# Optimization experiments

Hardware: AMD Instinct MI355X
Metric: run time of the kernel (lower is better)

## Reference

```python
import jax, jax.numpy as jnp
import numpy as np
import math

B, L, WIN, D, H, FF, NL, V, M = 16, 2048, 128, 512, 8, 2048, 3, 32000, 32
HD = D // H
EPS = 1e-5
RECON_W = 0.1

def _ln(x, g, b):
    m = x.mean(-1, keepdims=True)
    v = ((x - m) ** 2).mean(-1, keepdims=True)
    return (x - m) * jax.lax.rsqrt(v + EPS) * g + b

def _denoiser(x_t, t, motif, left, right, glob, time_proj_W, time_proj_b, cond_proj_W, cond_proj_b,
              qkv_W, qkv_b, attn_out_W, attn_out_b, ff1_W, ff1_b, ff2_W, ff2_b,
              ln1_g, ln1_b, ln2_g, ln2_b, out_W, out_b):
    half = D // 2
    freqs = jnp.exp(-math.log(10000.0) * jnp.arange(half) / (half - 1))
    a = t[:, None] * freqs[None, :]
    temb = jnp.concatenate([jnp.sin(a), jnp.cos(a)], -1) @ time_proj_W.T + time_proj_b
    x = x_t + temb[:, None, :]
    cond = jnp.concatenate([motif, left, right, glob], -1) @ cond_proj_W.T + cond_proj_b
    x = jnp.concatenate([cond[:, None, :], x], 1)
    S = x.shape[1]
    for i in range(NL):  # post-norm TransformerEncoderLayer, relu, no dropout (eval)
        qkv = x @ qkv_W[i].T + qkv_b[i]
        q, k, v = jnp.split(qkv, 3, axis=-1)
        q = q.reshape(B, S, H, HD); k = k.reshape(B, S, H, HD); v = v.reshape(B, S, H, HD)
        attn = jax.nn.softmax(jnp.einsum('bqhd,bkhd->bhqk', q, k) / math.sqrt(HD), axis=-1)
        ctx = jnp.einsum('bhqk,bkhd->bqhd', attn, v).reshape(B, S, D)
        x = _ln(x + ctx @ attn_out_W[i].T + attn_out_b[i], ln1_g[i], ln1_b[i])
        h = jax.nn.relu(x @ ff1_W[i].T + ff1_b[i]) @ ff2_W[i].T + ff2_b[i]
        x = _ln(x + h, ln2_g[i], ln2_b[i])
    return x[:, 1:, :] @ out_W.T + out_b

def setup_inputs():
    key = jax.random.key(0)
    ks = jax.random.split(key, 20)
    s = 0.02
    inp = {}
    inp['token_ids'] = jax.random.randint(ks[0], (B, L), 0, V)
    inp['motif_ids'] = jax.random.randint(ks[1], (B, M), 0, V)
    inp['motif_len'] = jax.random.randint(ks[2], (B,), 1, M + 1)
    inp['window_start'] = jax.random.randint(ks[3], (B,), 0, L - WIN)
    lens = jax.random.randint(ks[4], (B,), 1, WIN + 1).at[0].set(WIN)
    inp['window_end'] = inp['window_start'] + lens
    inp['t'] = jax.random.uniform(ks[5], (B,))
    inp['x0'] = jax.random.normal(ks[6], (B, WIN, D))
    inp['embed_table'] = jax.random.normal(ks[7], (V, D)) * s
    inp['decode_W'] = jax.random.normal(ks[8], (V, D)) * s
    inp['decode_b'] = jnp.zeros((V,))
    inp['adapter_W'] = jax.random.normal(ks[9], (D, D)) * s
    inp['adapter_b'] = jnp.zeros((D,))
    inp['time_proj_W'] = jax.random.normal(ks[10], (D, D)) * s
    inp['time_proj_b'] = jnp.zeros((D,))
    inp['cond_proj_W'] = jax.random.normal(ks[11], (D, 4 * D)) * s
    inp['cond_proj_b'] = jnp.zeros((D,))
    inp['qkv_W'] = jax.random.normal(ks[12], (NL, 3 * D, D)) * s
    inp['qkv_b'] = jnp.zeros((NL, 3 * D))
    inp['attn_out_W'] = jax.random.normal(ks[13], (NL, D, D)) * s
    inp['attn_out_b'] = jnp.zeros((NL, D))
    inp['ff1_W'] = jax.random.normal(ks[14], (NL, FF, D)) * s
    inp['ff1_b'] = jnp.zeros((NL, FF))
    inp['ff2_W'] = jax.random.normal(ks[15], (NL, D, FF)) * s
    inp['ff2_b'] = jnp.zeros((NL, D))
    inp['ln1_g'] = jnp.ones((NL, D)); inp['ln1_b'] = jnp.zeros((NL, D))
    inp['ln2_g'] = jnp.ones((NL, D)); inp['ln2_b'] = jnp.zeros((NL, D))
    inp['out_W'] = jax.random.normal(ks[16], (D, D)) * s
    inp['out_b'] = jnp.zeros((D,))
    return inp

def _forward(token_ids, motif_ids, motif_len, window_start, window_end, t, x0,
             embed_table, decode_W, decode_b, adapter_W, adapter_b, den):
    hidden = embed_table[token_ids]  # frozen backbone encode: [B, L, D]
    pos = jnp.arange(L)
    def pool(s, e):  # vectorized masked mean over region [s, e)
        m = ((pos[None, :] >= s[:, None]) & (pos[None, :] < e[:, None])).astype(hidden.dtype)
        return jnp.einsum('bl,bld->bd', m, hidden) / jnp.maximum(m.sum(1, keepdims=True), 1.0)
    left = pool(jnp.zeros_like(window_start), window_start)
    right = pool(window_end, jnp.full_like(window_end, L))
    glob = hidden.mean(1)
    memb = embed_table[motif_ids]
    mmask = (jnp.arange(M)[None, :] < motif_len[:, None]).astype(memb.dtype)
    motif = (memb * mmask[..., None]).sum(1) / jnp.maximum(motif_len.astype(memb.dtype), 1.0)[:, None]
    actual = jnp.clip(window_end - window_start, 0, WIN)
    win_mask = jnp.arange(WIN)[None, :] < actual[:, None]
    idx = jnp.clip(window_start[:, None] + jnp.arange(WIN)[None, :], 0, L - 1)
    x1 = jnp.take_along_axis(hidden, idx[:, :, None], axis=1) * win_mask[..., None]
    x_t = (1 - t[:, None, None]) * x0 + t[:, None, None] * x1
    target_v = x1 - x0
    pred_v = _denoiser(x_t, t, motif, left, right, glob, *den)
    valid = win_mask[..., None].astype(x1.dtype)
    vel = (((pred_v - target_v) ** 2) * valid).sum() / (jnp.maximum(valid.sum(), 1.0) * D)
    pred_x1 = x_t + (1 - t[:, None, None]) * pred_v
    logits = (pred_x1 @ adapter_W.T + adapter_b) @ decode_W.T + decode_b
    labels = jnp.where(win_mask, jnp.take_along_axis(token_ids, idx, axis=1), -100)
    lv = labels != -100
    logp = jax.nn.log_softmax(logits, axis=-1)
    picked = jnp.take_along_axis(logp, jnp.maximum(labels, 0)[..., None], axis=-1)[..., 0]
    recon = -(picked * lv).sum() / jnp.maximum(lv.sum(), 1)
    return vel + RECON_W * recon

def reference(token_ids, motif_ids, motif_len, window_start, window_end, t, x0,
              embed_table, decode_W, decode_b, adapter_W, adapter_b,
              time_proj_W, time_proj_b, cond_proj_W, cond_proj_b, qkv_W, qkv_b,
              attn_out_W, attn_out_b, ff1_W, ff1_b, ff2_W, ff2_b,
              ln1_g, ln1_b, ln2_g, ln2_b, out_W, out_b):
    den = (time_proj_W, time_proj_b, cond_proj_W, cond_proj_b, qkv_W, qkv_b,
           attn_out_W, attn_out_b, ff1_W, ff1_b, ff2_W, ff2_b,
           ln1_g, ln1_b, ln2_g, ln2_b, out_W, out_b)
    return _forward(token_ids, motif_ids, motif_len, window_start, window_end, t, x0,
                    embed_table, decode_W, decode_b, adapter_W, adapter_b, den)
```

## Files before the change

### kernel.cpp

```cpp
#include <hip/hip_runtime.h>
#include <hip/hip_bf16.h>
#include <math.h>

typedef __hip_bfloat16 bf16;

constexpr int cB = 16, cL = 2048, cWIN = 128, cD = 512, cH = 8, cFF = 2048;
constexpr int cNL = 3, cV = 32000, cM = 32;
constexpr int cHD = cD / cH;
constexpr int cS = cWIN + 1;
constexpr float cEPS = 1e-5f;
constexpr float cRECON_W = 0.1f;
constexpr int cNVT = cV / 128;

__device__ __forceinline__ float b2f(bf16 x) { return __bfloat162float(x); }

__device__ __forceinline__ float ldx(const void* p, size_t i, int f32) {
    return f32 ? ((const float*)p)[i]
               : __bfloat162float(((const bf16*)p)[i]);
}

__device__ __forceinline__ unsigned int f2bf(float f) {
    union { float f; unsigned int u; } v; v.f = f;
    unsigned int u = v.u + 0x7FFFu + ((v.u >> 16) & 1u);
    return u >> 16;
}

typedef short bf16x8 __attribute__((ext_vector_type(8)));
typedef float f32x4  __attribute__((ext_vector_type(4)));

__global__ void detect_kernel(const void* __restrict__ x0raw, int* __restrict__ flag)
{
    const unsigned short* h = (const unsigned short*)x0raw;
    int tid = threadIdx.x;
    int cnt = 0;
    for (int j = tid; j < 8192; j += 256) {
        unsigned short u = h[2 * j];
        int e = (u >> 7) & 0xFF;
        if (e >= 134) cnt++;
    }
    __shared__ int red[256];
    red[tid] = cnt; __syncthreads();
    for (int off = 128; off > 0; off >>= 1) {
        if (tid < off) red[tid] += red[tid + off];
        __syncthreads();
    }
    if (tid == 0) *flag = (red[0] > 400) ? 1 : 0;
}

__global__ __launch_bounds__(512) void pools_part_kernel(
    const int* __restrict__ tok, const int* __restrict__ wstart,
    const int* __restrict__ wend, const void* __restrict__ emb,
    float* __restrict__ part, const int* __restrict__ dflag)
{
    const int f32 = *dflag;
    int chunk = blockIdx.x;
    int b = blockIdx.y;
    int d = threadIdx.x;
    int ws_ = wstart[b], we_ = wend[b];
    float sl = 0.f, sr = 0.f, sg = 0.f;
    int l0 = chunk * 256;
    for (int l = l0; l < l0 + 256; ++l) {
        int t = tok[b * cL + l];
        float h = ldx(emb, (size_t)t * cD + d, f32);
        sg += h;
        if (l < ws_) sl += h;
        if (l >= we_) sr += h;
    }
    size_t base = ((size_t)(b * 8 + chunk)) * 3 * cD;
    part[base + d]            = sl;
    part[base + cD + d]       = sr;
    part[base + 2 * cD + d]   = sg;
}

__global__ __launch_bounds__(512) void pools_combine_kernel(
    const float* __restrict__ part, const int* __restrict__ mids,
    const int* __restrict__ mlen, const int* __restrict__ wstart,
    const int* __restrict__ wend, const void* __restrict__ emb,
    unsigned short* __restrict__ featb, const int* __restrict__ dflag)
{
    const int f32 = *dflag;
    int b = blockIdx.x;
    int d = threadIdx.x;
    int ws_ = wstart[b], we_ = wend[b];
    float sl = 0.f, sr = 0.f, sg = 0.f;
    for (int c = 0; c < 8; ++c) {
        size_t base = ((size_t)(b * 8 + c)) * 3 * cD;
        sl += part[base + d];
        sr += part[base + cD + d];
        sg += part[base + 2 * cD + d];
    }
    int ml = mlen[b];
    float sm = 0.f;
    for (int j = 0; j < cM; ++j) {
        if (j < ml) sm += ldx(emb, (size_t)mids[b * cM + j] * cD + d, f32);
    }
    unsigned short* fr = featb + (size_t)b * (4 * cD);
    fr[d]            = (unsigned short)f2bf(sm / fmaxf((float)ml, 1.f));
    fr[cD + d]       = (unsigned short)f2bf(sl / fmaxf((float)ws_, 1.f));
    fr[2 * cD + d]   = (unsigned short)f2bf(sr / fmaxf((float)(cL - we_), 1.f));
    fr[3 * cD + d]   = (unsigned short)f2bf(sg / (float)cL);
}

__global__ __launch_bounds__(512) void tf_kernel(
    const void* __restrict__ t_arr, unsigned short* __restrict__ tfbb,
    const int* __restrict__ dflag)
{
    const int f32 = *dflag;
    int b = blockIdx.x;
    int j = threadIdx.x;
    float t = ldx(t_arr, b, f32);
    const int half = cD / 2;
    float v;
    if (j < half) {
        float fr = expf(-logf(10000.f) * (float)j / (float)(half - 1));
        v = sinf(t * fr);
    } else {
        float fr = expf(-logf(10000.f) * (float)(j - half) / (float)(half - 1));
        v = cosf(t * fr);
    }
    tfbb[(size_t)b * cD + j] = (unsigned short)f2bf(v);
}

__global__ __launch_bounds__(512) void build_x_kernel(
    const int* __restrict__ tok, const int* __restrict__ wstart,
    const int* __restrict__ wend, const void* __restrict__ t_arr,
    const void* __restrict__ x0, const void* __restrict__ emb,
    const float* __restrict__ cond, const float* __restrict__ temb,
    float* __restrict__ x, unsigned short* __restrict__ xbf,
    float* __restrict__ x1, float* __restrict__ xt,
    const int* __restrict__ dflag)
{
    const int f32 = *dflag;
    int row = blockIdx.x;
    int b = row / cS, s = row % cS;
    int d = threadIdx.x;
    if (s == 0) {
        float cv = cond[b * cD + d];
        x[(size_t)row * cD + d] = cv;
        xbf[(size_t)row * cD + d] = (unsigned short)f2bf(cv);
        return;
    }
    int i = s - 1;
    int ws_ = wstart[b], we_ = wend[b];
    int actual = min(max(we_ - ws_, 0), cWIN);
    int idx = min(ws_ + i, cL - 1);
    float x1v = 0.f;
    if (i < actual) x1v = ldx(emb, (size_t)tok[b * cL + idx] * cD + d, f32);
    float t = ldx(t_arr, b, f32);
    float x0v = ldx(x0, ((size_t)b * cWIN + i) * cD + d, f32);
    float xtv = (1.f - t) * x0v + t * x1v;
    size_t ro = ((size_t)b * cWIN + i) * cD + d;
    x1[ro] = x1v;
    xt[ro] = xtv;
    float xv = xtv + temb[b * cD + d];
    x[(size_t)row * cD + d] = xv;
    xbf[(size_t)row * cD + d] = (unsigned short)f2bf(xv);
}

constexpr int GL2 = 72;
__global__ __launch_bounds__(256) void gemm_bf(
    const unsigned short* __restrict__ Abf, const void* __restrict__ Wb,
    size_t wOff, const void* __restrict__ biasb, size_t bOff,
    float* __restrict__ Cf, unsigned short* __restrict__ Cbf,
    int Mdim, int Ndim, int Kdim, int relu, int obf,
    const int* __restrict__ dflag)
{
    const int f32 = *dflag;
    const float* Wf = (const float*)Wb + wOff;
    const unsigned short* Wh = (const unsigned short*)Wb + wOff;
    __shared__ unsigned short As[2][64 * GL2];
    __shared__ unsigned short Bs[2][64 * GL2];
    const int tid = threadIdx.x;
    const int lane = tid & 63;
    const int wid = tid >> 6;
    const int wm = wid >> 1, wn = wid & 1;
    const int quad = lane >> 4, lm = lane & 15;
    const int m0 = blockIdx.y * 64;
    const int n0 = blockIdx.x * 64;

    f32x4 acc[2][2];
    #pragma unroll
    for (int i = 0; i < 2; ++i)
        #pragma unroll
        for (int j = 0; j < 2; ++j)
            acc[i][j] = (f32x4){0.f, 0.f, 0.f, 0.f};

    uint4 ra[2], rb[2];
    const int srow = tid >> 3;
    const int sc8  = (tid & 7) * 8;

    auto loadA = [&](int k0) {
        #pragma unroll
        for (int t = 0; t < 2; ++t) {
            int row = srow + t * 32;
            uint4 v = {0u, 0u, 0u, 0u};
            if (m0 + row < Mdim)
                v = *(const uint4*)(Abf + (size_t)(m0 + row) * Kdim + k0 + sc8);
            ra[t] = v;
        }
    };
    auto loadB = [&](int k0) {
        #pragma unroll
        for (int t = 0; t < 2; ++t) {
            int row = srow + t * 32;
            size_t g = (size_t)(n0 + row) * Kdim + k0 + sc8;
            if (f32) {
                float4 v0 = *(const float4*)(Wf + g);
                float4 v1 = *(const float4*)(Wf + g + 4);
                rb[t] = make_uint4(
                    f2bf(v0.x) | (f2bf(v0.y) << 16), f2bf(v0.z) | (f2bf(v0.w) << 16),
                    f2bf(v1.x) | (f2bf(v1.y) << 16), f2bf(v1.z) | (f2bf(v1.w) << 16));
            } else {
                rb[t] = *(const uint4*)(Wh + g);
            }
        }
    };

    loadA(0); loadB(0);
    const int nk = Kdim >> 6;
    for (int t = 0; t < nk; ++t) {
        const int buf = t & 1;
        #pragma unroll
        for (int u = 0; u < 2; ++u) {
            *(uint4*)(&As[buf][(srow + u * 32) * GL2 + sc8]) = ra[u];
            *(uint4*)(&Bs[buf][(srow + u * 32) * GL2 + sc8]) = rb[u];
        }
        __syncthreads();
        if (t + 1 < nk) { loadA((t + 1) * 64); loadB((t + 1) * 64); }
        #pragma unroll
        for (int kk = 0; kk < 2; ++kk) {
            bf16x8 a0 = *(const bf16x8*)(&As[buf][(wm * 32 + lm) * GL2 + kk * 32 + quad * 8]);
            bf16x8 a1 = *(const bf16x8*)(&As[buf][(wm * 32 + 16 + lm) * GL2 + kk * 32 + quad * 8]);
            bf16x8 b0 = *(const bf16x8*)(&Bs[buf][(wn * 32 + lm) * GL2 + kk * 32 + quad * 8]);
            bf16x8 b1 = *(const bf16x8*)(&Bs[buf][(wn * 32 + 16 + lm) * GL2 + kk * 32 + quad * 8]);
            acc[0][0] = __builtin_amdgcn_mfma_f32_16x16x32_bf16(a0, b0, acc[0][0], 0, 0, 0);
            acc[0][1] = __builtin_amdgcn_mfma_f32_16x16x32_bf16(a0, b1, acc[0][1], 0, 0, 0);
            acc[1][0] = __builtin_amdgcn_mfma_f32_16x16x32_bf16(a1, b0, acc[1][0], 0, 0, 0);
            acc[1][1] = __builtin_amdgcn_mfma_f32_16x16x32_bf16(a1, b1, acc[1][1], 0, 0, 0);
        }
    }

    #pragma unroll
    for (int in = 0; in < 2; ++in) {
        int gc = n0 + wn * 32 + in * 16 + lm;
        float bv = ldx(biasb, bOff + gc, f32);
        #pragma unroll
        for (int im = 0; im < 2; ++im) {
            #pragma unroll
            for (int r = 0; r < 4; ++r) {
                int gr = m0 + wm * 32 + im * 16 + quad * 4 + r;
                if (gr < Mdim) {
                    float v = acc[im][in][r] + bv;
                    if (relu) v = fmaxf(v, 0.f);
                    if (obf) Cbf[(size_t)gr * Ndim + gc] = (unsigned short)f2bf(v);
                    else     Cf[(size_t)gr * Ndim + gc] = v;
                }
            }
        }
    }
}

__global__ __launch_bounds__(256) void attn_mfma_kernel(
    const unsigned short* __restrict__ qkv, unsigned short* __restrict__ ctx)
{
    constexpr int SP = 160;
    constexpr int KP = 72;
    constexpr int VP = 168;
    const int h = blockIdx.x, b = blockIdx.y;
    const int tid = threadIdx.x;
    const int lane = tid & 63;
    const int wid = tid >> 6;
    const int quad = lane >> 4, lm = lane & 15;

    __shared__ unsigned short Ks[SP * KP];
    __shared__ unsigned short Vt[64 * VP];
    __shared__ unsigned short Pl[4 * 16 * VP];

    const unsigned short* base = qkv + (size_t)b * cS * (3 * cD) + h * cHD;

    for (int c = tid; c < SP * 8; c += 256) {
        int row = c >> 3, g = c & 7;
        uint4 v = {0u, 0u, 0u, 0u};
        if (row < cS)
            v = *(const uint4*)(base + (size_t)row * (3 * cD) + cD + g * 8);
        *(uint4*)(Ks + row * KP + g * 8) = v;
    }
    for (int c = tid; c < SP * 16; c += 256) {
        int key = c >> 4, d4 = c & 15;
        uint2 v = {0u, 0u};
        if (key < cS)
            v = *(const uint2*)(base + (size_t)key * (3 * cD) + 2 * cD + d4 * 4);
        Vt[(d4 * 4 + 0) * VP + key] = (unsigned short)(v.x & 0xFFFFu);
        Vt[(d4 * 4 + 1) * VP + key] = (unsigned short)(v.x >> 16);
        Vt[(d4 * 4 + 2) * VP + key] = (unsigned short)(v.y & 0xFFFFu);
        Vt[(d4 * 4 + 3) * VP + key] = (unsigned short)(v.y >> 16);
    }
    __syncthreads();

    unsigned short* Pw = Pl + wid * (16 * VP);

    for (int t = wid; t < 9; t += 4) {
        int qs = t * 16 + lm;
        bf16x8 aq[2];
        #pragma unroll
        for (int j = 0; j < 8; ++j) { aq[0][j] = 0; aq[1][j] = 0; }
        if (qs < cS) {
            const unsigned short* qrow = base + (size_t)qs * (3 * cD);
            aq[0] = *(const bf16x8*)(qrow + quad * 8);
            aq[1] = *(const bf16x8*)(qrow + 32 + quad * 8);
        }

        f32x4 sc[10];
        #pragma unroll
        for (int n = 0; n < 10; ++n) {
            sc[n] = (f32x4){0.f, 0.f, 0.f, 0.f};
            bf16x8 bk0 = *(const bf16x8*)(Ks + (n * 16 + lm) * KP + quad * 8);
            sc[n] = __builtin_amdgcn_mfma_f32_16x16x32_bf16(aq[0], bk0, sc[n], 0, 0, 0);
            bf16x8 bk1 = *(const bf16x8*)(Ks + (n * 16 + lm) * KP + 32 + quad * 8);
            sc[n] = __builtin_amdgcn_mfma_f32_16x16x32_bf16(aq[1], bk1, sc[n], 0, 0, 0);
        }

        #pragma unroll
        for (int r = 0; r < 4; ++r) {
            float mx = -3.0e38f;
            #pragma unroll
            for (int n = 0; n < 10; ++n) {
                float v = sc[n][r] * 0.125f;
                mx = fmaxf(mx, ((n * 16 + lm) < cS) ? v : -3.0e38f);
            }
            #pragma unroll
            for (int msk = 1; msk < 16; msk <<= 1)
                mx = fmaxf(mx, __shfl_xor(mx, msk));
            float p[10];
            float sum = 0.f;
            #pragma unroll
            for (int n = 0; n < 10; ++n) {
                float e = ((n * 16 + lm) < cS) ? expf(sc[n][r] * 0.125f - mx) : 0.f;
                p[n] = e; sum += e;
            }
            #pragma unroll
            for (int msk = 1; msk < 16; msk <<= 1)
                sum += __shfl_xor(sum, msk);
            float inv = 1.f / sum;
            unsigned short* pr = Pw + (quad * 4 + r) * VP + lm;
            #pragma unroll
            for (int n = 0; n < 10; ++n)
                pr[n * 16] = (unsigned short)f2bf(p[n] * inv);
        }

        asm volatile("s_waitcnt lgkmcnt(0)" ::: "memory");
        __builtin_amdgcn_sched_barrier(0);

        f32x4 o[4];
        #pragma unroll
        for (int j = 0; j < 4; ++j) o[j] = (f32x4){0.f, 0.f, 0.f, 0.f};
        #pragma unroll
        for (int ks = 0; ks < 5; ++ks) {
            bf16x8 ap = *(const bf16x8*)(Pw + lm * VP + ks * 32 + quad * 8);
            #pragma unroll
            for (int j = 0; j < 4; ++j) {
                bf16x8 bv = *(const bf16x8*)(Vt + (j * 16 + lm) * VP + ks * 32 + quad * 8);
                o[j] = __builtin_amdgcn_mfma_f32_16x16x32_bf16(ap, bv, o[j], 0, 0, 0);
            }
        }

        #pragma unroll
        for (int r = 0; r < 4; ++r) {
            int s_ = t * 16 + quad * 4 + r;
            if (s_ < cS) {
                unsigned short* orow = ctx + ((size_t)(b * cS + s_)) * cD + h * cHD;
                #pragma unroll
                for (int j = 0; j < 4; ++j)
                    orow[j * 16 + lm] = (unsigned short)f2bf(o[j][r]);
            }
        }
    }
}

__global__ __launch_bounds__(256) void resid_ln_kernel(
    float* __restrict__ x, const float* __restrict__ h,
    const void* __restrict__ g, const void* __restrict__ bta, size_t off,
    unsigned short* __restrict__ xbf, const int* __restrict__ dflag)
{
    const int f32 = *dflag;
    int row = blockIdx.x;
    int tid = threadIdx.x;
    __shared__ float red[256];
    float v[2];
    float s = 0.f;
    #pragma unroll
    for (int j = 0; j < 2; ++j) {
        int d = tid + j * 256;
        v[j] = x[(size_t)row * cD + d] + h[(size_t)row * cD + d];
        s += v[j];
    }
    red[tid] = s; __syncthreads();
    for (int o = 128; o > 0; o >>= 1) {
        if (tid < o) red[tid] += red[tid + o];
        __syncthreads();
    }
    float mean = red[0] / (float)cD;
    __syncthreads();
    float vs = 0.f;
    #pragma unroll
    for (int j = 0; j < 2; ++j) { float dd = v[j] - mean; vs += dd * dd; }
    red[tid] = vs; __syncthreads();
    for (int o = 128; o > 0; o >>= 1) {
        if (tid < o) red[tid] += red[tid + o];
        __syncthreads();
    }
    float rs = rsqrtf(red[0] / (float)cD + cEPS);
    #pragma unroll
    for (int j = 0; j < 2; ++j) {
        int d = tid + j * 256;
        float ov = (v[j] - mean) * rs * ldx(g, off + d, f32) + ldx(bta, off + d, f32);
        x[(size_t)row * cD + d] = ov;
        xbf[(size_t)row * cD + d] = (unsigned short)f2bf(ov);
    }
}

__global__ __launch_bounds__(512) void copy_xs_kernel(
    const float* __restrict__ x, unsigned short* __restrict__ xs)
{
    int row = blockIdx.x;
    int b = row / cWIN, i = row % cWIN;
    int d = threadIdx.x;
    xs[(size_t)row * cD + d] =
        (unsigned short)f2bf(x[((size_t)(b * cS + 1 + i)) * cD + d]);
}

__global__ __launch_bounds__(256) void vel_kernel(
    const float* __restrict__ pv, const float* __restrict__ x1,
    const void* __restrict__ x0, const int* __restrict__ wstart,
    const int* __restrict__ wend, float* __restrict__ velpart,
    const int* __restrict__ dflag)
{
    const int f32 = *dflag;
    int row = blockIdx.x;
    int b = row / cWIN, i = row % cWIN;
    int tid = threadIdx.x;
    int actual = min(max(wend[b] - wstart[b], 0), cWIN);
    if (i >= actual) {
        if (tid == 0) velpart[row] = 0.f;
        return;
    }
    __shared__ float red[256];
    float s = 0.f;
    for (int d = tid; d < cD; d += 256) {
        size_t o = (size_t)row * cD + d;
        float tv = x1[o] - ldx(x0, o, f32);
        float diff = pv[o] - tv;
        s += diff * diff;
    }
    red[tid] = s; __syncthreads();
    for (int off = 128; off > 0; off >>= 1) {
        if (tid < off) red[tid] += red[tid + off];
        __syncthreads();
    }
    if (tid == 0) velpart[row] = red[0];
}

__global__ __launch_bounds__(512) void predx1_kernel(
    const float* __restrict__ xt, const float* __restrict__ pv,
    const void* __restrict__ t_arr, unsigned short* __restrict__ outp,
    const int* __restrict__ dflag)
{
    const int f32 = *dflag;
    int row = blockIdx.x;
    int b = row / cWIN;
    int d = threadIdx.x;
    float t = ldx(t_arr, b, f32);
    size_t o = (size_t)row * cD + d;
    outp[o] = (unsigned short)f2bf(xt[o] + (1.f - t) * pv[o]);
}

__global__ void labels_kernel(
    const int* __restrict__ tok, const int* __restrict__ wstart,
    const int* __restrict__ wend, int* __restrict__ labels)
{
    int r = blockIdx.x * 256 + threadIdx.x;
    if (r >= cB * cWIN) return;
    int b = r / cWIN, i = r % cWIN;
    int ws_ = wstart[b], we_ = wend[b];
    int actual = min(max(we_ - ws_, 0), cWIN);
    labels[r] = (i < actual) ? tok[b * cL + min(ws_ + i, cL - 1)] : -1;
}

__global__ __launch_bounds__(256) void cvt_w_kernel(
    const void* __restrict__ Wsrc, unsigned short* __restrict__ dst,
    const int* __restrict__ dflag)
{
    if (!*dflag) return;
    const float4* src = (const float4*)Wsrc;
    size_t n4 = (size_t)cV * cD / 4;
    for (size_t i = (size_t)blockIdx.x * 256 + threadIdx.x; i < n4;
         i += (size_t)gridDim.x * 256) {
        float4 v = src[i];
        unsigned int p0 = f2bf(v.x) | (f2bf(v.y) << 16);
        unsigned int p1 = f2bf(v.z) | (f2bf(v.w) << 16);
        ((uint2*)dst)[i] = make_uint2(p0, p1);
    }
}

constexpr int GLDS = 40;
__global__ __launch_bounds__(256) void decode_mfma2_kernel(
    const unsigned short* __restrict__ hbf, const unsigned short* __restrict__ wbf,
    const void* __restrict__ dW, const void* __restrict__ db,
    const int* __restrict__ labels,
    float* __restrict__ pm, float* __restrict__ ps, float* __restrict__ lab,
    const int* __restrict__ dflag)
{
    const int f32 = *dflag;
    const unsigned short* Wsrc = f32 ? wbf : (const unsigned short*)dW;
    const int bid = blockIdx.x;
    const int xcd = bid & 7;
    const int local = bid >> 3;
    const int nt = xcd * 32 + (local >> 4);
    const int mt = local & 15;
    if (nt >= cNVT) return;
    const int m0 = mt * 128, n0 = nt * 128;

    __shared__ unsigned short As[128 * GLDS];
    __shared__ unsigned short Bs[128 * GLDS];
    const int tid = threadIdx.x;
    const int lane = tid & 63;
    const int wid = tid >> 6;
    const int wm = wid >> 1, wn = wid & 1;
    const int quad = lane >> 4, lm = lane & 15;

    f32x4 acc[4][4];
    #pragma unroll
    for (int i = 0; i < 4; ++i)
        #pragma unroll
        for (int j = 0; j < 4; ++j)
            acc[i][j] = (f32x4){0.f, 0.f, 0.f, 0.f};

    for (int k0 = 0; k0 < cD; k0 += 32) {
        #pragma unroll
        for (int t = 0; t < 2; ++t) {
            int idx = tid + t * 256;
            int row = idx >> 2, c = idx & 3;
            uint4 v = *(const uint4*)(hbf + (size_t)(m0 + row) * cD + k0 + c * 8);
            *(uint4*)(As + row * GLDS + c * 8) = v;
        }
        #pragma unroll
        for (int t = 0; t < 2; ++t) {
            int idx = tid + t * 256;
            int row = idx >> 2, c = idx & 3;
            uint4 v = *(const uint4*)(Wsrc + (size_t)(n0 + row) * cD + k0 + c * 8);
            *(uint4*)(Bs + row * GLDS + c * 8) = v;
        }
        __syncthreads();
        bf16x8 af[4], bfr[4];
        #pragma unroll
        for (int im = 0; im < 4; ++im) {
            int row = wm * 64 + im * 16 + lm;
            af[im] = *(const bf16x8*)(As + row * GLDS + quad * 8);
        }
        #pragma unroll
        for (int in = 0; in < 4; ++in) {
            int row = wn * 64 + in * 16 + lm;
            bfr[in] = *(const bf16x8*)(Bs + row * GLDS + quad * 8);
        }
        #pragma unroll
        for (int im = 0; im < 4; ++im)
            #pragma unroll
            for (int in = 0; in < 4; ++in)
                acc[im][in] = __builtin_amdgcn_mfma_f32_16x16x32_bf16(
                    af[im], bfr[in], acc[im][in], 0, 0, 0);
        __syncthreads();
    }

    float bv[4];
    #pragma unroll
    for (int in = 0; in < 4; ++in)
        bv[in] = ldx(db, n0 + wn * 64 + in * 16 + lm, f32);
    #pragma unroll
    for (int im = 0; im < 4; ++im)
        #pragma unroll
        for (int in = 0; in < 4; ++in)
            #pragma unroll
            for (int r = 0; r < 4; ++r)
                acc[im][in][r] += bv[in];

    #pragma unroll
    for (int im = 0; im < 4; ++im) {
        #pragma unroll
        for (int r = 0; r < 4; ++r) {
            int gr = m0 + wm * 64 + im * 16 + quad * 4 + r;
            int lb = labels[gr];
            #pragma unroll
            for (int in = 0; in < 4; ++in) {
                int col = n0 + wn * 64 + in * 16 + lm;
                if (lb == col) lab[gr] = acc[im][in][r];
            }
        }
    }

    __shared__ float red[128][33];
    __shared__ float mrow[128];
    #pragma unroll
    for (int im = 0; im < 4; ++im) {
        #pragma unroll
        for (int r = 0; r < 4; ++r) {
            int rl = wm * 64 + im * 16 + quad * 4 + r;
            float mx = acc[im][0][r];
            #pragma unroll
            for (int in = 1; in < 4; ++in) mx = fmaxf(mx, acc[im][in][r]);
            red[rl][wn * 16 + lm] = mx;
        }
    }
    __syncthreads();
    if (tid < 128) {
        float mx = red[tid][0];
        #pragma unroll
        for (int t = 1; t < 32; ++t) mx = fmaxf(mx, red[tid][t]);
        mrow[tid] = mx;
    }
    __syncthreads();
    #pragma unroll
    for (int im = 0; im < 4; ++im) {
        #pragma unroll
        for (int r = 0; r < 4; ++r) {
            int rl = wm * 64 + im * 16 + quad * 4 + r;
            float m_ = mrow[rl];
            float s = 0.f;
            #pragma unroll
            for (int in = 0; in < 4; ++in) s += expf(acc[im][in][r] - m_);
            red[rl][wn * 16 + lm] = s;
        }
    }
    __syncthreads();
    if (tid < 128) {
        float s = red[tid][0];
        #pragma unroll
        for (int t = 1; t < 32; ++t) s += red[tid][t];
        int gr = m0 + tid;
        pm[(size_t)gr * cNVT + nt] = mrow[tid];
        ps[(size_t)gr * cNVT + nt] = s;
    }
}

__global__ __launch_bounds__(256) void decode_mfma_kernel(
    const unsigned short* __restrict__ hbf, const void* __restrict__ dW,
    const void* __restrict__ db, const int* __restrict__ labels,
    float* __restrict__ pm, float* __restrict__ ps, float* __restrict__ lab,
    const int* __restrict__ dflag)
{
    const int f32 = *dflag;
    const float* Wf = (const float*)dW;
    const unsigned short* Wh = (const unsigned short*)dW;
    __shared__ unsigned short As[128 * GLDS];
    __shared__ unsigned short Bs[128 * GLDS];
    const int tid = threadIdx.x;
    const int lane = tid & 63;
    const int wid = tid >> 6;
    const int wm = wid >> 1, wn = wid & 1;
    const int quad = lane >> 4, lm = lane & 15;
    const int nt = blockIdx.x;
    const int mt = blockIdx.y;
    const int m0 = mt * 128, n0 = nt * 128;

    f32x4 acc[4][4];
    #pragma unroll
    for (int i = 0; i < 4; ++i)
        #pragma unroll
        for (int j = 0; j < 4; ++j)
            acc[i][j] = (f32x4){0.f, 0.f, 0.f, 0.f};

    for (int k0 = 0; k0 < cD; k0 += 32) {
        #pragma unroll
        for (int t = 0; t < 2; ++t) {
            int idx = tid + t * 256;
            int row = idx >> 2, c = idx & 3;
            uint4 v = *(const uint4*)(hbf + (size_t)(m0 + row) * cD + k0 + c * 8);
            *(uint4*)(As + row * GLDS + c * 8) = v;
        }
        #pragma unroll
        for (int t = 0; t < 4; ++t) {
            int chunk = tid + t * 256;
            int row = chunk >> 3;
            int kc = (chunk & 7) * 4;
            size_t gro = (size_t)(n0 + row) * cD + k0 + kc;
            if (f32) {
                float4 v = *(const float4*)(Wf + gro);
                unsigned int p0 = f2bf(v.x) | (f2bf(v.y) << 16);
                unsigned int p1 = f2bf(v.z) | (f2bf(v.w) << 16);
                *(uint2*)(Bs + row * GLDS + kc) = make_uint2(p0, p1);
            } else {
                *(uint2*)(Bs + row * GLDS + kc) = *(const uint2*)(Wh + gro);
            }
        }
        __syncthreads();
        bf16x8 af[4], bfr[4];
        #pragma unroll
        for (int im = 0; im < 4; ++im) {
            int row = wm * 64 + im * 16 + lm;
            af[im] = *(const bf16x8*)(As + row * GLDS + quad * 8);
        }
        #pragma unroll
        for (int in = 0; in < 4; ++in) {
            int row = wn * 64 + in * 16 + lm;
            bfr[in] = *(const bf16x8*)(Bs + row * GLDS + quad * 8);
        }
        #pragma unroll
        for (int im = 0; im < 4; ++im)
            #pragma unroll
            for (int in = 0; in < 4; ++in)
                acc[im][in] = __builtin_amdgcn_mfma_f32_16x16x32_bf16(
                    af[im], bfr[in], acc[im][in], 0, 0, 0);
        __syncthreads();
    }

    float bv[4];
    #pragma unroll
    for (int in = 0; in < 4; ++in)
        bv[in] = ldx(db, n0 + wn * 64 + in * 16 + lm, f32);
    #pragma unroll
    for (int im = 0; im < 4; ++im)
        #pragma unroll
        for (int in = 0; in < 4; ++in)
            #pragma unroll
            for (int r = 0; r < 4; ++r)
                acc[im][in][r] += bv[in];

    #pragma unroll
    for (int im = 0; im < 4; ++im) {
        #pragma unroll
        for (int r = 0; r < 4; ++r) {
            int gr = m0 + wm * 64 + im * 16 + quad * 4 + r;
            int lb = labels[gr];
            #pragma unroll
            for (int in = 0; in < 4; ++in) {
                int col = n0 + wn * 64 + in * 16 + lm;
                if (lb == col) lab[gr] = acc[im][in][r];
            }
        }
    }

    __shared__ float red[128][33];
    __shared__ float mrow[128];
    #pragma unroll
    for (int im = 0; im < 4; ++im) {
        #pragma unroll
        for (int r = 0; r < 4; ++r) {
            int rl = wm * 64 + im * 16 + quad * 4 + r;
            float mx = acc[im][0][r];
            #pragma unroll
            for (int in = 1; in < 4; ++in) mx = fmaxf(mx, acc[im][in][r]);
            red[rl][wn * 16 + lm] = mx;
        }
    }
    __syncthreads();
    if (tid < 128) {
        float mx = red[tid][0];
        #pragma unroll
        for (int t = 1; t < 32; ++t) mx = fmaxf(mx, red[tid][t]);
        mrow[tid] = mx;
    }
    __syncthreads();
    #pragma unroll
    for (int im = 0; im < 4; ++im) {
        #pragma unroll
        for (int r = 0; r < 4; ++r) {
            int rl = wm * 64 + im * 16 + quad * 4 + r;
            float m_ = mrow[rl];
            float s = 0.f;
            #pragma unroll
            for (int in = 0; in < 4; ++in) s += expf(acc[im][in][r] - m_);
            red[rl][wn * 16 + lm] = s;
        }
    }
    __syncthreads();
    if (tid < 128) {
        float s = red[tid][0];
        #pragma unroll
        for (int t = 1; t < 32; ++t) s += red[tid][t];
        int gr = m0 + tid;
        pm[(size_t)gr * cNVT + nt] = mrow[tid];
        ps[(size_t)gr * cNVT + nt] = s;
    }
}

__global__ __launch_bounds__(64) void lse_reduce_kernel(
    const float* __restrict__ pm, const float* __restrict__ ps,
    const float* __restrict__ lab, const int* __restrict__ labels,
    float* __restrict__ logppart)
{
    int r = blockIdx.x;
    int tid = threadIdx.x;
    if (labels[r] < 0) {
        if (tid == 0) logppart[r] = 0.f;
        return;
    }
    float m = -1e30f;
    for (int c = tid; c < cNVT; c += 64) m = fmaxf(m, pm[(size_t)r * cNVT + c]);
    for (int off = 32; off > 0; off >>= 1) m = fmaxf(m, __shfl_down(m, off));
    m = __shfl(m, 0);
    float s = 0.f;
    for (int c = tid; c < cNVT; c += 64)
        s += ps[(size_t)r * cNVT + c] * expf(pm[(size_t)r * cNVT + c] - m);
    for (int off = 32; off > 0; off >>= 1) s += __shfl_down(s, off);
    if (tid == 0) logppart[r] = lab[r] - (m + logf(s));
}

__global__ __launch_bounds__(256) void finalize_kernel(
    const float* __restrict__ velpart, const float* __restrict__ logppart,
    const int* __restrict__ wstart, const int* __restrict__ wend,
    void* __restrict__ out, const int* __restrict__ dflag)
{
    const int f32 = *dflag;
    __shared__ float r1[256], r2[256];
    int tid = threadIdx.x;
    float s1 = 0.f, s2 = 0.f;
    for (int r = tid; r < cB * cWIN; r += 256) {
        s1 += velpart[r];
        s2 += logppart[r];
    }
    r1[tid] = s1; r2[tid] = s2; __syncthreads();
    for (int off = 128; off > 0; off >>= 1) {
        if (tid < off) { r1[tid] += r1[tid + off]; r2[tid] += r2[tid + off]; }
        __syncthreads();
    }
    if (tid == 0) {
        float cnt = 0.f;
        for (int b = 0; b < cB; ++b)
            cnt += (float)min(max(wend[b] - wstart[b], 0), cWIN);
        cnt = fmaxf(cnt, 1.f);
        float vel = r1[0] / (cnt * (float)cD);
        float recon = -r2[0] / cnt;
        float loss = vel + cRECON_W * recon;
        if (f32) ((float*)out)[0] = loss;
        else     ((bf16*)out)[0] = __float2bfloat16(loss);
    }
}

extern "C" void kernel_launch(void* const* d_in, const int* in_sizes, int n_in,
                              void* d_out, int out_size, void* d_ws, size_t ws_size,
                              hipStream_t stream) {
    const int*  token_ids    = (const int*)d_in[0];
    const int*  motif_ids    = (const int*)d_in[1];
    const int*  motif_len    = (const int*)d_in[2];
    const int*  window_start = (const int*)d_in[3];
    const int*  window_end   = (const int*)d_in[4];
    const void* t_arr        = d_in[5];
    const void* x0           = d_in[6];
    const void* embed_table  = d_in[7];
    const void* decode_W     = d_in[8];
    const void* decode_b     = d_in[9];
    const void* adapter_W    = d_in[10];
    const void* adapter_b    = d_in[11];
    const void* time_proj_W  = d_in[12];
    const void* time_proj_b  = d_in[13];
    const void* cond_proj_W  = d_in[14];
    const void* cond_proj_b  = d_in[15];
    const void* qkv_W        = d_in[16];
    const void* qkv_b        = d_in[17];
    const void* attn_out_W   = d_in[18];
    const void* attn_out_b   = d_in[19];
    const void* ff1_W        = d_in[20];
    const void* ff1_b        = d_in[21];
    const void* ff2_W        = d_in[22];
    const void* ff2_b        = d_in[23];
    const void* ln1_g        = d_in[24];
    const void* ln1_b        = d_in[25];
    const void* ln2_g        = d_in[26];
    const void* ln2_b        = d_in[27];
    const void* out_W        = d_in[28];
    const void* out_b        = d_in[29];

    float* w = (float*)d_ws;
    const size_t SZ_X   = (size_t)cB * cS * cD;
    const size_t SZ_BA  = (size_t)cB * cS * cFF;
    const size_t SZ_ROW = (size_t)cB * cWIN * cD;
    float* x     = w;
    float* bufA  = x + SZ_X;
    float* bufB  = bufA + SZ_BA;
    float* bufC  = bufB + SZ_X;
    float* x1b   = bufC + SZ_X;
    float* xtb   = x1b + SZ_ROW;
    float* pvb   = xtb + SZ_ROW;
    float* h2b   = pvb + SZ_ROW;
    float* feat  = h2b + SZ_ROW;
    float* tfb   = feat + (size_t)cB * 4 * cD;
    float* cond  = tfb + (size_t)cB * cD;
    float* temb  = cond + (size_t)cB * cD;
    float* velpart = temb + (size_t)cB * cD;
    float* logppart = velpart + (size_t)cB * cWIN;
    int*   dflag = (int*)(logppart + (size_t)cB * cWIN);
    float* wsend = (float*)(dflag + 16);
    unsigned short* wbf = (unsigned short*)wsend;

    const size_t need_bytes = ((char*)wsend - (char*)d_ws)
                            + (size_t)cV * cD * sizeof(unsigned short) + 256;
    const bool fast_decode = ws_size >= need_bytes;

    const int Wrows = cB * cWIN;
    const int Mrows = cB * cS;

    unsigned short* xbf    = (unsigned short*)h2b;
    unsigned short* featbf = xbf + (size_t)Mrows * cD;
    unsigned short* tfbbf  = featbf + (size_t)cB * 4 * cD;
    unsigned short* qkvbf  = (unsigned short*)bufA;
    unsigned short* ff1bf  = (unsigned short*)bufA;
    unsigned short* ctxbf  = (unsigned short*)bufB;
    unsigned short* xsbf   = (unsigned short*)(bufA + (size_t)3 * 1024 * 1024);
    unsigned short* px1bf  = xsbf;
    unsigned short* hbf    = (unsigned short*)bufC;

    float* pm  = bufA;
    float* ps  = pm + (size_t)Wrows * cNVT;
    float* lab = ps + (size_t)Wrows * cNVT;
    int*   labels = (int*)(lab + Wrows);
    float* poolspart = bufC;

    auto gemm = [&](const unsigned short* A, const void* W, size_t wOff,
                    const void* bias, size_t bOff, float* Cf, unsigned short* Cbf,
                    int M_, int N_, int K_, int relu, int obf) {
        dim3 grid(N_ / 64, (M_ + 63) / 64);
        gemm_bf<<<grid, 256, 0, stream>>>(A, W, wOff, bias, bOff, Cf, Cbf,
                                          M_, N_, K_, relu, obf, dflag);
    };

    detect_kernel<<<1, 256, 0, stream>>>(x0, dflag);
    if (fast_decode)
        cvt_w_kernel<<<4096, 256, 0, stream>>>(decode_W, wbf, dflag);
    pools_part_kernel<<<dim3(8, cB), cD, 0, stream>>>(token_ids, window_start,
        window_end, embed_table, poolspart, dflag);
    pools_combine_kernel<<<cB, cD, 0, stream>>>(poolspart, motif_ids, motif_len,
        window_start, window_end, embed_table, featbf, dflag);
    tf_kernel<<<cB, cD, 0, stream>>>(t_arr, tfbbf, dflag);
    gemm(featbf, cond_proj_W, 0, cond_proj_b, 0, cond, nullptr, cB, cD, 4 * cD, 0, 0);
    gemm(tfbbf, time_proj_W, 0, time_proj_b, 0, temb, nullptr, cB, cD, cD, 0, 0);
    build_x_kernel<<<Mrows, cD, 0, stream>>>(token_ids, window_start, window_end,
        t_arr, x0, embed_table, cond, temb, x, xbf, x1b, xtb, dflag);

    for (int i = 0; i < cNL; ++i) {
        gemm(xbf, qkv_W, (size_t)i * 3 * cD * cD, qkv_b, (size_t)i * 3 * cD,
             nullptr, qkvbf, Mrows, 3 * cD, cD, 0, 1);
        attn_mfma_kernel<<<dim3(cH, cB), 256, 0, stream>>>(qkvbf, ctxbf);
        gemm(ctxbf, attn_out_W, (size_t)i * cD * cD, attn_out_b, (size_t)i * cD,
             bufC, nullptr, Mrows, cD, cD, 0, 0);
        resid_ln_kernel<<<Mrows, 256, 0, stream>>>(x, bufC, ln1_g, ln1_b,
             (size_t)i * cD, xbf, dflag);
        gemm(xbf, ff1_W, (size_t)i * cFF * cD, ff1_b, (size_t)i * cFF,
             nullptr, ff1bf, Mrows, cFF, cD, 1, 1);
        gemm(ff1bf, ff2_W, (size_t)i * cD * cFF, ff2_b, (size_t)i * cD,
             bufC, nullptr, Mrows, cD, cFF, 0, 0);
        resid_ln_kernel<<<Mrows, 256, 0, stream>>>(x, bufC, ln2_g, ln2_b,
             (size_t)i * cD, xbf, dflag);
    }

    copy_xs_kernel<<<Wrows, cD, 0, stream>>>(x, xsbf);
    gemm(xsbf, out_W, 0, out_b, 0, pvb, nullptr, Wrows, cD, cD, 0, 0);
    vel_kernel<<<Wrows, 256, 0, stream>>>(pvb, x1b, x0, window_start, window_end,
        velpart, dflag);
    predx1_kernel<<<Wrows, cD, 0, stream>>>(xtb, pvb, t_arr, px1bf, dflag);
    gemm(px1bf, adapter_W, 0, adapter_b, 0, nullptr, hbf, Wrows, cD, cD, 0, 1);

    labels_kernel<<<(Wrows + 255) / 256, 256, 0, stream>>>(
        token_ids, window_start, window_end, labels);
    if (fast_decode) {
        decode_mfma2_kernel<<<4096, 256, 0, stream>>>(
            hbf, wbf, decode_W, decode_b, labels, pm, ps, lab, dflag);
    } else {
        decode_mfma_kernel<<<dim3(cNVT, Wrows / 128), 256, 0, stream>>>(
            hbf, decode_W, decode_b, labels, pm, ps, lab, dflag);
    }
    lse_reduce_kernel<<<Wrows, 64, 0, stream>>>(pm, ps, lab, labels, logppart);

    finalize_kernel<<<1, 256, 0, stream>>>(velpart, logppart,
        window_start, window_end, d_out, dflag);
}
```

Baseline: 972.3 us.

## Swizzle GEMM LDS, use direct global-to-LDS loads in decode, fuse tail kernels

The generic GEMM gets an XOR swizzle on its LDS tile layout, which is meant to cut bank conflicts. It also gains a row-remap mode that reads the window rows straight from xbf, so the copy_xs kernel can be dropped. The decode GEMM now loads tiles with global_load_lds into a compact swizzled shared buffer and reuses that buffer for the reduction scratch, which lowers LDS footprint and the register staging traffic. The vel and predx1 kernels are merged into one pass so pv is read once.

```diff
diff --git a/kernel.cpp b/kernel.cpp
--- a/kernel.cpp
+++ b/kernel.cpp
@@ -23,6 +23,12 @@
     union { float f; unsigned int u; } v; v.f = f;
     unsigned int u = v.u + 0x7FFFu + ((v.u >> 16) & 1u);
     return u >> 16;
+}
+
+__device__ __forceinline__ void glds16(const unsigned short* g, unsigned short* l) {
+    __builtin_amdgcn_global_load_lds(
+        (const __attribute__((address_space(1))) void*)g,
+        (__attribute__((address_space(3))) void*)l, 16, 0, 0);
 }
 
 typedef short bf16x8 __attribute__((ext_vector_type(8)));
@@ -162,7 +168,7 @@
     const unsigned short* __restrict__ Abf, const void* __restrict__ Wb,
     size_t wOff, const void* __restrict__ biasb, size_t bOff,
     float* __restrict__ Cf, unsigned short* __restrict__ Cbf,
-    int Mdim, int Ndim, int Kdim, int relu, int obf,
+    int Mdim, int Ndim, int Kdim, int relu, int obf, int amap,
     const int* __restrict__ dflag)
 {
     const int f32 = *dflag;
@@ -188,14 +194,19 @@
     uint4 ra[2], rb[2];
     const int srow = tid >> 3;
     const int sc8  = (tid & 7) * 8;
+    const int ssw  = ((tid & 7) ^ ((tid >> 3) & 7)) * 8;
+    const int lmm  = lm & 7;
 
     auto loadA = [&](int k0) {
         #pragma unroll
         for (int t = 0; t < 2; ++t) {
-            int row = srow + t * 32;
+            int r0 = m0 + srow + t * 32;
             uint4 v = {0u, 0u, 0u, 0u};
-            if (m0 + row < Mdim)
-                v = *(const uint4*)(Abf + (size_t)(m0 + row) * Kdim + k0 + sc8);
+            if (r0 < Mdim) {
+                size_t ar = amap ? ((size_t)(r0 >> 7) * cS + 1 + (r0 & 127))
+                                 : (size_t)r0;
+                v = *(const uint4*)(Abf + ar * Kdim + k0 + sc8);
+            }
             ra[t] = v;
         }
     };
@@ -222,17 +233,18 @@
         const int buf = t & 1;
         #pragma unroll
         for (int u = 0; u < 2; ++u) {
-            *(uint4*)(&As[buf][(srow + u * 32) * GL2 + sc8]) = ra[u];
-            *(uint4*)(&Bs[buf][(srow + u * 32) * GL2 + sc8]) = rb[u];
+            *(uint4*)(&As[buf][(srow + u * 32) * GL2 + ssw]) = ra[u];
+            *(uint4*)(&Bs[buf][(srow + u * 32) * GL2 + ssw]) = rb[u];
         }
         __syncthreads();
         if (t + 1 < nk) { loadA((t + 1) * 64); loadB((t + 1) * 64); }
         #pragma unroll
         for (int kk = 0; kk < 2; ++kk) {
-            bf16x8 a0 = *(const bf16x8*)(&As[buf][(wm * 32 + lm) * GL2 + kk * 32 + quad * 8]);
-            bf16x8 a1 = *(const bf16x8*)(&As[buf][(wm * 32 + 16 + lm) * GL2 + kk * 32 + quad * 8]);
-            bf16x8 b0 = *(const bf16x8*)(&Bs[buf][(wn * 32 + lm) * GL2 + kk * 32 + quad * 8]);
-            bf16x8 b1 = *(const bf16x8*)(&Bs[buf][(wn * 32 + 16 + lm) * GL2 + kk * 32 + quad * 8]);
+            const int sl = ((kk * 4 + quad) ^ lmm) * 8;
+            bf16x8 a0 = *(const bf16x8*)(&As[buf][(wm * 32 + lm) * GL2 + sl]);
+            bf16x8 a1 = *(const bf16x8*)(&As[buf][(wm * 32 + 16 + lm) * GL2 + sl]);
+            bf16x8 b0 = *(const bf16x8*)(&Bs[buf][(wn * 32 + lm) * GL2 + sl]);
+            bf16x8 b1 = *(const bf16x8*)(&Bs[buf][(wn * 32 + 16 + lm) * GL2 + sl]);
             acc[0][0] = __builtin_amdgcn_mfma_f32_16x16x32_bf16(a0, b0, acc[0][0], 0, 0, 0);
             acc[0][1] = __builtin_amdgcn_mfma_f32_16x16x32_bf16(a0, b1, acc[0][1], 0, 0, 0);
             acc[1][0] = __builtin_amdgcn_mfma_f32_16x16x32_bf16(a1, b0, acc[1][0], 0, 0, 0);
@@ -419,59 +431,35 @@
     }
 }
 
-__global__ __launch_bounds__(512) void copy_xs_kernel(
-    const float* __restrict__ x, unsigned short* __restrict__ xs)
-{
-    int row = blockIdx.x;
-    int b = row / cWIN, i = row % cWIN;
-    int d = threadIdx.x;
-    xs[(size_t)row * cD + d] =
-        (unsigned short)f2bf(x[((size_t)(b * cS + 1 + i)) * cD + d]);
-}
-
-__global__ __launch_bounds__(256) void vel_kernel(
-    const float* __restrict__ pv, const float* __restrict__ x1,
-    const void* __restrict__ x0, const int* __restrict__ wstart,
-    const int* __restrict__ wend, float* __restrict__ velpart,
-    const int* __restrict__ dflag)
+__global__ __launch_bounds__(512) void predvel_kernel(
+    const float* __restrict__ xt, const float* __restrict__ pv,
+    const float* __restrict__ x1, const void* __restrict__ x0,
+    const void* __restrict__ t_arr, const int* __restrict__ wstart,
+    const int* __restrict__ wend, unsigned short* __restrict__ px1,
+    float* __restrict__ velpart, const int* __restrict__ dflag)
 {
     const int f32 = *dflag;
     int row = blockIdx.x;
-    int b = row / cWIN, i = row % cWIN;
-    int tid = threadIdx.x;
-    int actual = min(max(wend[b] - wstart[b], 0), cWIN);
-    if (i >= actual) {
-        if (tid == 0) velpart[row] = 0.f;
-        return;
-    }
-    __shared__ float red[256];
-    float s = 0.f;
-    for (int d = tid; d < cD; d += 256) {
-        size_t o = (size_t)row * cD + d;
-        float tv = x1[o] - ldx(x0, o, f32);
-        float diff = pv[o] - tv;
-        s += diff * diff;
-    }
-    red[tid] = s; __syncthreads();
-    for (int off = 128; off > 0; off >>= 1) {
-        if (tid < off) red[tid] += red[tid + off];
-        __syncthreads();
-    }
-    if (tid == 0) velpart[row] = red[0];
-}
-
-__global__ __launch_bounds__(512) void predx1_kernel(
-    const float* __restrict__ xt, const float* __restrict__ pv,
-    const void* __restrict__ t_arr, unsigned short* __restrict__ outp,
-    const int* __restrict__ dflag)
-{
-    const int f32 = *dflag;
-    int row = blockIdx.x;
-    int b = row / cWIN;
+    int b = row >> 7, i = row & 127;
     int d = threadIdx.x;
     float t = ldx(t_arr, b, f32);
     size_t o = (size_t)row * cD + d;
-    outp[o] = (unsigned short)f2bf(xt[o] + (1.f - t) * pv[o]);
+    float pvv = pv[o];
+    px1[o] = (unsigned short)f2bf(xt[o] + (1.f - t) * pvv);
+    int actual = min(max(wend[b] - wstart[b], 0), cWIN);
+    float s = 0.f;
+    if (i < actual) {
+        float tv = x1[o] - ldx(x0, o, f32);
+        float diff = pvv - tv;
+        s = diff * diff;
+    }
+    __shared__ float red[512];
+    red[d] = s; __syncthreads();
+    for (int off = 256; off > 0; off >>= 1) {
+        if (d < off) red[d] += red[d + off];
+        __syncthreads();
+    }
+    if (d == 0) velpart[row] = red[0];
 }
 
 __global__ void labels_kernel(
@@ -502,7 +490,6 @@
     }
 }
 
-constexpr int GLDS = 40;
 __global__ __launch_bounds__(256) void decode_mfma2_kernel(
     const unsigned short* __restrict__ hbf, const unsigned short* __restrict__ wbf,
     const void* __restrict__ dW, const void* __restrict__ db,
@@ -520,14 +507,23 @@
     if (nt >= cNVT) return;
     const int m0 = mt * 128, n0 = nt * 128;
 
-    __shared__ unsigned short As[128 * GLDS];
-    __shared__ unsigned short Bs[128 * GLDS];
+    __shared__ __align__(16) char smem[17408];
+    unsigned short* As = (unsigned short*)smem;
+    unsigned short* Bs = As + 4096;
+
     const int tid = threadIdx.x;
     const int lane = tid & 63;
     const int wid = tid >> 6;
     const int wm = wid >> 1, wn = wid & 1;
     const int quad = lane >> 4, lm = lane & 15;
 
+    const int grow  = lane >> 2;
+    const int gslot = (lane & 3) ^ ((lane >> 3) & 3);
+    const int rslot = (quad ^ ((lm >> 1) & 3)) * 8;
+
+    const unsigned short* gA = hbf  + (size_t)(m0 + wid * 32 + grow) * cD + gslot * 8;
+    const unsigned short* gB = Wsrc + (size_t)(n0 + wid * 32 + grow) * cD + gslot * 8;
+
     f32x4 acc[4][4];
     #pragma unroll
     for (int i = 0; i < 4; ++i)
@@ -537,31 +533,18 @@
 
     for (int k0 = 0; k0 < cD; k0 += 32) {
         #pragma unroll
-        for (int t = 0; t < 2; ++t) {
-            int idx = tid + t * 256;
-            int row = idx >> 2, c = idx & 3;
-            uint4 v = *(const uint4*)(hbf + (size_t)(m0 + row) * cD + k0 + c * 8);
-            *(uint4*)(As + row * GLDS + c * 8) = v;
-        }
-        #pragma unroll
-        for (int t = 0; t < 2; ++t) {
-            int idx = tid + t * 256;
-            int row = idx >> 2, c = idx & 3;
-            uint4 v = *(const uint4*)(Wsrc + (size_t)(n0 + row) * cD + k0 + c * 8);
-            *(uint4*)(Bs + row * GLDS + c * 8) = v;
+        for (int c = 0; c < 2; ++c) {
+            glds16(gA + (size_t)c * 16 * cD + k0, As + (wid * 2 + c) * 512);
+            glds16(gB + (size_t)c * 16 * cD + k0, Bs + (wid * 2 + c) * 512);
         }
         __syncthreads();
         bf16x8 af[4], bfr[4];
         #pragma unroll
-        for (int im = 0; im < 4; ++im) {
-            int row = wm * 64 + im * 16 + lm;
-            af[im] = *(const bf16x8*)(As + row * GLDS + quad * 8);
-        }
-        #pragma unroll
-        for (int in = 0; in < 4; ++in) {
-            int row = wn * 64 + in * 16 + lm;
-            bfr[in] = *(const bf16x8*)(Bs + row * GLDS + quad * 8);
-        }
+        for (int im = 0; im < 4; ++im)
+            af[im] = *(const bf16x8*)(As + (wm * 64 + im * 16 + lm) * 32 + rslot);
+        #pragma unroll
+        for (int in = 0; in < 4; ++in)
+            bfr[in] = *(const bf16x8*)(Bs + (wn * 64 + in * 16 + lm) * 32 + rslot);
         #pragma unroll
         for (int im = 0; im < 4; ++im)
             #pragma unroll
@@ -597,8 +580,8 @@
         }
     }
 
-    __shared__ float red[128][33];
-    __shared__ float mrow[128];
+    float (*red)[33] = (float(*)[33])smem;
+    float* mrow = (float*)(smem + 16896);
     #pragma unroll
     for (int im = 0; im < 4; ++im) {
         #pragma unroll
@@ -641,6 +624,7 @@
     }
 }
 
+constexpr int GLDS = 40;
 __global__ __launch_bounds__(256) void decode_mfma_kernel(
     const unsigned short* __restrict__ hbf, const void* __restrict__ dW,
     const void* __restrict__ db, const int* __restrict__ labels,
@@ -904,8 +888,7 @@
     unsigned short* qkvbf  = (unsigned short*)bufA;
     unsigned short* ff1bf  = (unsigned short*)bufA;
     unsigned short* ctxbf  = (unsigned short*)bufB;
-    unsigned short* xsbf   = (unsigned short*)(bufA + (size_t)3 * 1024 * 1024);
-    unsigned short* px1bf  = xsbf;
+    unsigned short* px1bf  = (unsigned short*)(bufA + (size_t)3 * 1024 * 1024);
     unsigned short* hbf    = (unsigned short*)bufC;
 
     float* pm  = bufA;
@@ -916,10 +899,10 @@
 
     auto gemm = [&](const unsigned short* A, const void* W, size_t wOff,
                     const void* bias, size_t bOff, float* Cf, unsigned short* Cbf,
-                    int M_, int N_, int K_, int relu, int obf) {
+                    int M_, int N_, int K_, int relu, int obf, int amap) {
         dim3 grid(N_ / 64, (M_ + 63) / 64);
         gemm_bf<<<grid, 256, 0, stream>>>(A, W, wOff, bias, bOff, Cf, Cbf,
-                                          M_, N_, K_, relu, obf, dflag);
+                                          M_, N_, K_, relu, obf, amap, dflag);
     };
 
     detect_kernel<<<1, 256, 0, stream>>>(x0, dflag);
@@ -930,33 +913,31 @@
     pools_combine_kernel<<<cB, cD, 0, stream>>>(poolspart, motif_ids, motif_len,
         window_start, window_end, embed_table, featbf, dflag);
     tf_kernel<<<cB, cD, 0, stream>>>(t_arr, tfbbf, dflag);
-    gemm(featbf, cond_proj_W, 0, cond_proj_b, 0, cond, nullptr, cB, cD, 4 * cD, 0, 0);
-    gemm(tfbbf, time_proj_W, 0, time_proj_b, 0, temb, nullptr, cB, cD, cD, 0, 0);
+    gemm(featbf, cond_proj_W, 0, cond_proj_b, 0, cond, nullptr, cB, cD, 4 * cD, 0, 0, 0);
+    gemm(tfbbf, time_proj_W, 0, time_proj_b, 0, temb, nullptr, cB, cD, cD, 0, 0, 0);
     build_x_kernel<<<Mrows, cD, 0, stream>>>(token_ids, window_start, window_end,
         t_arr, x0, embed_table, cond, temb, x, xbf, x1b, xtb, dflag);
 
     for (int i = 0; i < cNL; ++i) {
         gemm(xbf, qkv_W, (size_t)i * 3 * cD * cD, qkv_b, (size_t)i * 3 * cD,
-             nullptr, qkvbf, Mrows, 3 * cD, cD, 0, 1);
+             nullptr, qkvbf, Mrows, 3 * cD, cD, 0, 1, 0);
         attn_mfma_kernel<<<dim3(cH, cB), 256, 0, stream>>>(qkvbf, ctxbf);
         gemm(ctxbf, attn_out_W, (size_t)i * cD * cD, attn_out_b, (size_t)i * cD,
-             bufC, nullptr, Mrows, cD, cD, 0, 0);
+             bufC, nullptr, Mrows, cD, cD, 0, 0, 0);
         resid_ln_kernel<<<Mrows, 256, 0, stream>>>(x, bufC, ln1_g, ln1_b,
              (size_t)i * cD, xbf, dflag);
         gemm(xbf, ff1_W, (size_t)i * cFF * cD, ff1_b, (size_t)i * cFF,
-             nullptr, ff1bf, Mrows, cFF, cD, 1, 1);
+             nullptr, ff1bf, Mrows, cFF, cD, 1, 1, 0);
         gemm(ff1bf, ff2_W, (size_t)i * cD * cFF, ff2_b, (size_t)i * cD,
-             bufC, nullptr, Mrows, cD, cFF, 0, 0);
+             bufC, nullptr, Mrows, cD, cFF, 0, 0, 0);
         resid_ln_kernel<<<Mrows, 256, 0, stream>>>(x, bufC, ln2_g, ln2_b,
              (size_t)i * cD, xbf, dflag);
     }
 
-    copy_xs_kernel<<<Wrows, cD, 0, stream>>>(x, xsbf);
-    gemm(xsbf, out_W, 0, out_b, 0, pvb, nullptr, Wrows, cD, cD, 0, 0);
-    vel_kernel<<<Wrows, 256, 0, stream>>>(pvb, x1b, x0, window_start, window_end,
-        velpart, dflag);
-    predx1_kernel<<<Wrows, cD, 0, stream>>>(xtb, pvb, t_arr, px1bf, dflag);
-    gemm(px1bf, adapter_W, 0, adapter_b, 0, nullptr, hbf, Wrows, cD, cD, 0, 1);
+    gemm(xbf, out_W, 0, out_b, 0, pvb, nullptr, Wrows, cD, cD, 0, 0, 1);
+    predvel_kernel<<<Wrows, 512, 0, stream>>>(xtb, pvb, x1b, x0, t_arr,
+        window_start, window_end, px1bf, velpart, dflag);
+    gemm(px1bf, adapter_W, 0, adapter_b, 0, nullptr, hbf, Wrows, cD, cD, 0, 1, 0);
 
     labels_kernel<<<(Wrows + 255) / 256, 256, 0, stream>>>(
         token_ids, window_start, window_end, labels);
```

Result: no change. 964.5 us (-0.8%).
